# Performance work log

Hardware: AMD Instinct MI355X
Metric: run time of the kernel (lower is better)

## Reference

```python
import jax, jax.numpy as jnp
import numpy as np

B, S, D, H = 4, 2048, 1024, 16
HD = D // H  # head size = 64

def setup_inputs() -> dict:
    key = jax.random.key(0)
    ks = jax.random.split(key, 9)
    s = 1.0 / np.sqrt(D)
    inp = {"x": jax.random.normal(ks[0], (B, S, D), dtype=jnp.float32)}
    for i, n in enumerate(["q", "k", "v", "o"]):
        inp[f"W{n}"] = jax.random.uniform(ks[1 + 2 * i], (D, D), minval=-s, maxval=s, dtype=jnp.float32)
        inp[f"b{n}"] = jax.random.uniform(ks[2 + 2 * i], (D,), minval=-s, maxval=s, dtype=jnp.float32)
    return inp

def reference(x, Wq, bq, Wk, bk, Wv, bv, Wo, bo):
    b, s, d = x.shape
    # project and split heads: [b, h, s, hd]
    def heads(y):
        return y.reshape(b, s, H, HD).transpose(0, 2, 1, 3)
    q = heads(x @ Wq.T + bq)
    k = heads(x @ Wk.T + bk)
    v = heads(x @ Wv.T + bv)
    scores = jnp.einsum('bhqd,bhkd->bhqk', q, k) / jnp.sqrt(jnp.float32(HD))
    attn = jax.nn.softmax(scores, axis=-1)
    ctx = jnp.einsum('bhqk,bhkd->bhqd', attn, v)
    ctx = ctx.transpose(0, 2, 1, 3).reshape(b, s, d)
    return ctx @ Wo.T + bo
```

## Files before the change

### kernel.cpp

```cpp
#include <hip/hip_runtime.h>
#include <hip/hip_bf16.h>

typedef __bf16 bf16;
typedef __bf16 bf16x8 __attribute__((ext_vector_type(8)));
typedef __bf16 bf16x4 __attribute__((ext_vector_type(4)));
typedef float f32x4 __attribute__((ext_vector_type(4)));
typedef float f32x16 __attribute__((ext_vector_type(16)));
typedef unsigned int u32;
typedef u32 u32x4 __attribute__((ext_vector_type(4)));

#define B_ 4
#define S_ 2048
#define D_ 1024
#define H_ 16
#define HD_ 64
#define QKLD 2048
#define LOG2E 1.4426950408889634f

static __device__ __forceinline__ f32x4 mfma16(bf16x8 a, bf16x8 b, f32x4 c) {
  return __builtin_amdgcn_mfma_f32_16x16x32_bf16(a, b, c, 0, 0, 0);
}
static __device__ __forceinline__ f32x16 mfma32(bf16x8 a, bf16x8 b, f32x16 c) {
  return __builtin_amdgcn_mfma_f32_32x32x16_bf16(a, b, c, 0, 0, 0);
}
static __device__ __forceinline__ void gload_lds16(const void* g, void* l) {
  __builtin_amdgcn_global_load_lds(
      (const __attribute__((address_space(1))) void*)g,
      (__attribute__((address_space(3))) void*)l, 16, 0, 0);
}
static __device__ __forceinline__ u32 pack2(float lo, float hi) {
  union { bf16 h[2]; u32 u; } un;
  un.h[0] = (bf16)lo; un.h[1] = (bf16)hi;
  return un.u;
}

__global__ void cvt_kernel(const float* __restrict__ in, bf16* __restrict__ out, int n4) {
  int i = blockIdx.x * blockDim.x + threadIdx.x;
  const int stride = gridDim.x * blockDim.x;
  for (; i < n4; i += stride) {
    float4 v = reinterpret_cast<const float4*>(in)[i];
    bf16x4 o;
    o[0] = (bf16)v.x; o[1] = (bf16)v.y; o[2] = (bf16)v.z; o[3] = (bf16)v.w;
    reinterpret_cast<bf16x4*>(out)[i] = o;
  }
}
__global__ void cvtw_kernel(const float* __restrict__ w0, const float* __restrict__ w1,
                            const float* __restrict__ w2, const float* __restrict__ w3,
                            bf16* __restrict__ o0, bf16* __restrict__ o1,
                            bf16* __restrict__ o2, bf16* __restrict__ o3, int n4) {
  const float* in = blockIdx.y == 0 ? w0 : blockIdx.y == 1 ? w1 : blockIdx.y == 2 ? w2 : w3;
  bf16* out = blockIdx.y == 0 ? o0 : blockIdx.y == 1 ? o1 : blockIdx.y == 2 ? o2 : o3;
  const int i = blockIdx.x * blockDim.x + threadIdx.x;
  float4 v = reinterpret_cast<const float4*>(in)[i];
  bf16x4 o;
  o[0] = (bf16)v.x; o[1] = (bf16)v.y; o[2] = (bf16)v.z; o[3] = (bf16)v.w;
  reinterpret_cast<bf16x4*>(out)[i] = o;
}

template<bool OUT_BF16, bool BIAS_ROW>
__global__ __launch_bounds__(256, 2)
void gemm3(const bf16* __restrict__ A, const bf16* __restrict__ W,
           const float* __restrict__ bias, void* __restrict__ Cout,
           int M, int N, int K, float scale) {
  __shared__ __align__(16) char lds[73728];
  const int tid = threadIdx.x;
  const int wave = tid >> 6;
  const int lane = tid & 63;
  const int g = lane >> 4, r16 = lane & 15;
  const unsigned nwgx = gridDim.x;
  const unsigned nwg = nwgx * gridDim.y;
  unsigned lid = blockIdx.x + nwgx * blockIdx.y;
  unsigned swz = (lid & 7) * (nwg >> 3) + (lid >> 3);
  const int m0 = (int)(swz / nwgx) * 128, n0 = (int)(swz % nwgx) * 256;
  const int wm = (wave >> 1) * 64, wn = (wave & 1) * 128;

  f32x4 acc[4][8] = {};

  const int arow0 = tid >> 2;
  const int acol = ((tid & 3) ^ ((tid >> 3) & 3)) * 8;
  const int wdst = wave * 1024;
  const int nkt = K >> 5;

  auto stage = [&](int bi, int t) {
    char* buf = lds + bi * 24576;
    const int kb = t << 5;
#pragma unroll
    for (int q = 0; q < 2; ++q)
      gload_lds16(&A[(size_t)(m0 + q * 64 + arow0) * K + kb + acol],
                  buf + q * 4096 + wdst);
#pragma unroll
    for (int q = 0; q < 4; ++q)
      gload_lds16(&W[(size_t)(n0 + q * 64 + arow0) * K + kb + acol],
                  buf + 8192 + q * 4096 + wdst);
  };

  stage(0, 0);
  stage(1, 1);
  int cur = 0;

  for (int t = 0; t < nkt; ++t) {
    if (t + 1 < nkt) asm volatile("s_waitcnt vmcnt(6)" ::: "memory");
    else             asm volatile("s_waitcnt vmcnt(0)" ::: "memory");
    __builtin_amdgcn_s_barrier();
    int nx2 = cur + 2; if (nx2 >= 3) nx2 -= 3;
    if (t + 2 < nkt) stage(nx2, t + 2);

    const char* bufA = lds + cur * 24576;
    const char* bufB = bufA + 8192;
    bf16x8 af[4], bfr[8];
#pragma unroll
    for (int i = 0; i < 4; ++i) {
      const int ra = wm + i * 16 + r16;
      af[i] = *reinterpret_cast<const bf16x8*>(
          bufA + ra * 64 + ((g ^ ((ra >> 1) & 3)) << 4));
    }
#pragma unroll
    for (int j = 0; j < 8; ++j) {
      const int rb = wn + j * 16 + r16;
      bfr[j] = *reinterpret_cast<const bf16x8*>(
          bufB + rb * 64 + ((g ^ ((rb >> 1) & 3)) << 4));
    }
    __builtin_amdgcn_s_setprio(1);
#pragma unroll
    for (int i = 0; i < 4; ++i)
#pragma unroll
      for (int j = 0; j < 8; ++j)
        acc[i][j] = mfma16(af[i], bfr[j], acc[i][j]);
    __builtin_amdgcn_s_setprio(0);
    cur = (cur + 1 == 3) ? 0 : cur + 1;
  }

#pragma unroll
  for (int i = 0; i < 4; ++i) {
#pragma unroll
    for (int j = 0; j < 8; ++j) {
      const int col = n0 + wn + j * 16 + r16;
      float bcol = BIAS_ROW ? 0.f : bias[col];
#pragma unroll
      for (int r = 0; r < 4; ++r) {
        const int row = m0 + wm + i * 16 + g * 4 + r;
        const float bv = BIAS_ROW ? bias[row] : bcol;
        const float v = (acc[i][j][r] + bv) * scale;
        if (OUT_BF16)
          reinterpret_cast<bf16*>(Cout)[(size_t)row * N + col] = (bf16)v;
        else
          reinterpret_cast<float*>(Cout)[(size_t)row * N + col] = v;
      }
    }
  }
}

__global__ __launch_bounds__(256, 2)
void gemm_qkv(const bf16* __restrict__ X, const bf16* __restrict__ Wqk,
              const bf16* __restrict__ Wv,
              const float* __restrict__ bq, const float* __restrict__ bk,
              const float* __restrict__ bv,
              bf16* __restrict__ QKout, bf16* __restrict__ VTout) {
  __shared__ __align__(16) char lds[49152];
  const int tid = threadIdx.x;
  const int wave = tid >> 6;
  const int lane = tid & 63;
  const int g = lane >> 4, r16 = lane & 15;
  const int K = 1024;
  const unsigned lid = blockIdx.x;
  const unsigned swz = (lid & 7) * (1536 >> 3) + (lid >> 3);
  const bool isQK = swz < 1024;
  int m0, n0;
  const bf16 *Aptr, *Wptr;
  if (isQK) {
    m0 = (int)(swz >> 4) * 128;
    n0 = (int)(swz & 15) * 128;
    Aptr = X; Wptr = Wqk;
  } else {
    const unsigned v = swz - 1024;
    m0 = (int)(v >> 6) * 128;
    n0 = (int)(v & 63) * 128;
    Aptr = Wv; Wptr = X;
  }
  const int wm = (wave >> 1) * 64, wn = (wave & 1) * 64;

  f32x4 acc[4][4] = {};

  const int nkt = K >> 5;

  auto stage = [&](int bi, int t) {
    char* buf = lds + bi * 16384;
    const int kb = t << 5;
#pragma unroll
    for (int l = 0; l < 2; ++l) {
      const int s = tid + l * 256;
      const int row = s >> 2;
      const int col = ((s & 3) ^ ((s >> 3) & 3)) * 8;
      gload_lds16(&Aptr[(size_t)(m0 + row) * K + kb + col], buf + wave * 1024 + l * 4096);
      gload_lds16(&Wptr[(size_t)(n0 + row) * K + kb + col], buf + 8192 + wave * 1024 + l * 4096);
    }
  };

  stage(0, 0);
  stage(1, 1);
  int cur = 0;

  for (int t = 0; t < nkt; ++t) {
    if (t + 1 < nkt) asm volatile("s_waitcnt vmcnt(4)" ::: "memory");
    else             asm volatile("s_waitcnt vmcnt(0)" ::: "memory");
    __builtin_amdgcn_s_barrier();
    int nx2 = cur + 2; if (nx2 >= 3) nx2 -= 3;
    if (t + 2 < nkt) stage(nx2, t + 2);

    const char* bufA = lds + cur * 16384;
    const char* bufB = bufA + 8192;
    bf16x8 af[4], bfr[4];
#pragma unroll
    for (int i = 0; i < 4; ++i) {
      const int ra = wm + i * 16 + r16;
      af[i] = *reinterpret_cast<const bf16x8*>(
          bufA + ra * 64 + ((g ^ ((ra >> 1) & 3)) << 4));
      const int rb = wn + i * 16 + r16;
      bfr[i] = *reinterpret_cast<const bf16x8*>(
          bufB + rb * 64 + ((g ^ ((rb >> 1) & 3)) << 4));
    }
    __builtin_amdgcn_s_setprio(1);
#pragma unroll
    for (int i = 0; i < 4; ++i)
#pragma unroll
      for (int j = 0; j < 4; ++j)
        acc[i][j] = mfma16(af[i], bfr[j], acc[i][j]);
    __builtin_amdgcn_s_setprio(0);
    cur = (cur + 1 == 3) ? 0 : cur + 1;
  }

  if (isQK) {
#pragma unroll
    for (int i = 0; i < 4; ++i) {
#pragma unroll
      for (int j = 0; j < 4; ++j) {
        const int col = n0 + wn + j * 16 + r16;
        const bool isQ = col < 1024;
        const float bb = isQ ? bq[col] : bk[col - 1024];
        const float sc = isQ ? 0.125f * LOG2E : 1.0f;
#pragma unroll
        for (int r = 0; r < 4; ++r) {
          const int row = m0 + wm + i * 16 + g * 4 + r;
          QKout[(size_t)row * QKLD + col] = (bf16)((acc[i][j][r] + bb) * sc);
        }
      }
    }
  } else {
#pragma unroll
    for (int i = 0; i < 4; ++i) {
#pragma unroll
      for (int j = 0; j < 4; ++j) {
        const int col = n0 + wn + j * 16 + r16;
#pragma unroll
        for (int r = 0; r < 4; ++r) {
          const int row = m0 + wm + i * 16 + g * 4 + r;
          VTout[(size_t)row * (B_ * S_) + col] = (bf16)(acc[i][j][r] + bv[row]);
        }
      }
    }
  }
}

#define VMB(N) do { asm volatile("s_waitcnt vmcnt(" #N ")" ::: "memory"); \
                    __builtin_amdgcn_s_barrier(); } while (0)

__global__ __launch_bounds__(256, 2)
void attn_kernel(const bf16* __restrict__ QK, const bf16* __restrict__ Vt,
                 bf16* __restrict__ CTX) {
  const unsigned nwg = gridDim.x * gridDim.y;
  const unsigned lid = blockIdx.x + gridDim.x * blockIdx.y;
  const unsigned swzid = (lid & 7) * (nwg >> 3) + (lid >> 3);
  const int bh = (int)(swzid >> 3);
  const int q0 = (int)(swzid & 7) * 256;
  const int h = bh & (H_ - 1), b = bh >> 4;
  const int tid = threadIdx.x, wave = tid >> 6, lane = tid & 63;
  const int l32 = lane & 31, hi = lane >> 5;

  const bf16* Qb  = QK + ((size_t)b * S_) * QKLD + h * HD_;
  const bf16* Kb  = QK + ((size_t)b * S_) * QKLD + 1024 + h * HD_;
  const bf16* Vtb = Vt + (size_t)(h * HD_) * (B_ * S_) + b * S_;

  __shared__ __align__(16) char lds[49152];
  char* const kb0 = lds;             char* const vb0 = lds + 24576;
  char* const kb1 = lds + 8192;      char* const vb1 = lds + 32768;
  char* const kb2 = lds + 16384;     char* const vb2 = lds + 40960;

  const int qbase = q0 + wave * 64;
  bf16x8 qf0[4], qf1[4];
#pragma unroll
  for (int ks = 0; ks < 4; ++ks) {
    qf0[ks] = *reinterpret_cast<const bf16x8*>(&Qb[(size_t)(qbase + l32) * QKLD + ks * 16 + hi * 8]);
    qf1[ks] = *reinterpret_cast<const bf16x8*>(&Qb[(size_t)(qbase + 32 + l32) * QKLD + ks * 16 + hi * 8]);
  }

  bf16x8 onesf;
#pragma unroll
  for (int j = 0; j < 8; ++j) onesf[j] = (bf16)1.0f;

  f32x16 ctx00 = {}, ctx01 = {}, ctx10 = {}, ctx11 = {};
  f32x16 lacc0 = {}, lacc1 = {};

  const int krow0 = wave * 16 + (lane >> 3);
  const int xs = ((lane & 7) ^ (lane >> 3)) * 8;
  const int stoff = wave * 2048;
  const int swl = (l32 & 7) << 4;
  int coa[4];
#pragma unroll
  for (int ks = 0; ks < 4; ++ks) coa[ks] = (ks * 32 + hi * 16) ^ swl;
  const int rA = l32 * 128, rB = (32 + l32) * 128;

  const bf16* Kst = Kb  + (size_t)krow0 * QKLD + xs;
  const bf16* Vst = Vtb + (size_t)krow0 * (B_ * S_) + xs;

  auto stage = [&](char* kd, char* vd) {
    gload_lds16(Kst,                  kd + stoff);
    gload_lds16(Kst + 8 * QKLD,       kd + stoff + 1024);
    gload_lds16(Vst,                  vd + stoff);
    gload_lds16(Vst + 8 * (B_ * S_),  vd + stoff + 1024);
    Kst += 64 * QKLD;
    Vst += 64;
  };

  auto expack = [&](const f32x16& s, u32* w) {
#pragma unroll
    for (int a = 0; a < 4; ++a)
#pragma unroll
      for (int c = 0; c < 2; ++c)
        w[2 * a + c] = pack2(__builtin_amdgcn_exp2f(s[4 * a + 2 * c]),
                             __builtin_amdgcn_exp2f(s[4 * a + 2 * c + 1]));
  };

  auto compute = [&](const char* bK, const char* bV) {
    bf16x8 kf0[4], kf1[4];
#pragma unroll
    for (int ks = 0; ks < 4; ++ks) {
      kf0[ks] = *reinterpret_cast<const bf16x8*>(bK + rA + coa[ks]);
      kf1[ks] = *reinterpret_cast<const bf16x8*>(bK + rB + coa[ks]);
    }
    const f32x16 z = {};
    f32x16 s00, s01;
    __builtin_amdgcn_s_setprio(1);
    s00 = mfma32(kf0[0], qf0[0], z);
    s01 = mfma32(kf1[0], qf0[0], z);
#pragma unroll
    for (int ks = 1; ks < 4; ++ks) {
      s00 = mfma32(kf0[ks], qf0[ks], s00);
      s01 = mfma32(kf1[ks], qf0[ks], s01);
    }
    __builtin_amdgcn_s_setprio(0);
    u32 w00[8], w01[8];
    expack(s00, w00); expack(s01, w01);
    f32x16 s10, s11;
    __builtin_amdgcn_s_setprio(1);
    s10 = mfma32(kf0[0], qf1[0], z);
    s11 = mfma32(kf1[0], qf1[0], z);
#pragma unroll
    for (int ks = 1; ks < 4; ++ks) {
      s10 = mfma32(kf0[ks], qf1[ks], s10);
      s11 = mfma32(kf1[ks], qf1[ks], s11);
    }
    __builtin_amdgcn_s_setprio(0);
    u32 w10[8], w11[8];
    expack(s10, w10); expack(s11, w11);
    bf16x8 vf0[4], vf1[4];
#pragma unroll
    for (int ksp = 0; ksp < 4; ++ksp) {
      vf0[ksp] = *reinterpret_cast<const bf16x8*>(bV + rA + coa[ksp]);
      vf1[ksp] = *reinterpret_cast<const bf16x8*>(bV + rB + coa[ksp]);
    }
#pragma unroll
    for (int m = 0; m < 2; ++m) {
      const u32* wlo = m ? w10 : w00;
      const u32* whi = m ? w11 : w01;
      f32x16& la = m ? lacc1 : lacc0;
      f32x16& c0 = m ? ctx10 : ctx00;
      f32x16& c1 = m ? ctx11 : ctx01;
#pragma unroll
      for (int T = 0; T < 2; ++T) {
        const u32* w = T ? whi : wlo;
#pragma unroll
        for (int k1 = 0; k1 < 2; ++k1) {
          auto rAp = __builtin_amdgcn_permlane32_swap((int)w[4 * k1 + 0], (int)w[4 * k1 + 2], false, false);
          auto rBp = __builtin_amdgcn_permlane32_swap((int)w[4 * k1 + 1], (int)w[4 * k1 + 3], false, false);
          u32x4 fw;
          fw[0] = (u32)rAp[0]; fw[1] = (u32)rBp[0]; fw[2] = (u32)rAp[1]; fw[3] = (u32)rBp[1];
          const bf16x8 pa = __builtin_bit_cast(bf16x8, fw);
          const int ksp = 2 * T + k1;
          __builtin_amdgcn_s_setprio(1);
          la = mfma32(pa, onesf, la);
          c0 = mfma32(pa, vf0[ksp], c0);
          c1 = mfma32(pa, vf1[ksp], c1);
          __builtin_amdgcn_s_setprio(0);
        }
      }
    }
  };

  stage(kb0, vb0);
  stage(kb1, vb1);

  for (int u = 0; u < 10; ++u) {
    VMB(4); stage(kb2, vb2); compute(kb0, vb0);
    VMB(4); stage(kb0, vb0); compute(kb1, vb1);
    VMB(4); stage(kb1, vb1); compute(kb2, vb2);
  }
  VMB(4); compute(kb0, vb0);
  VMB(0); compute(kb1, vb1);
  __syncthreads();

  char* Cw = lds + wave * 8192;
#pragma unroll
  for (int rg = 0; rg < 16; ++rg) {
    const int ql = (rg & 3) + 8 * (rg >> 2) + 4 * hi;
    const int swq = (ql & 7) << 4;
    {
      const float inv = 1.0f / lacc0[rg];
      *reinterpret_cast<bf16*>(Cw + ql * 128 + ((l32 * 2) ^ swq)) = (bf16)(ctx00[rg] * inv);
      *reinterpret_cast<bf16*>(Cw + ql * 128 + ((64 + l32 * 2) ^ swq)) = (bf16)(ctx01[rg] * inv);
    }
    {
      const float inv = 1.0f / lacc1[rg];
      *reinterpret_cast<bf16*>(Cw + (32 + ql) * 128 + ((l32 * 2) ^ swq)) = (bf16)(ctx10[rg] * inv);
      *reinterpret_cast<bf16*>(Cw + (32 + ql) * 128 + ((64 + l32 * 2) ^ swq)) = (bf16)(ctx11[rg] * inv);
    }
  }
  asm volatile("" ::: "memory");
#pragma unroll
  for (int i = 0; i < 8; ++i) {
    const int s = i * 64 + lane;
    const int row = s >> 3, cs = (s & 7) * 16;
    bf16x8 v = *reinterpret_cast<const bf16x8*>(Cw + row * 128 + (cs ^ ((row & 7) << 4)));
    *reinterpret_cast<bf16x8*>(
        &CTX[(size_t)(b * S_ + q0 + wave * 64 + row) * D_ + h * HD_ + cs / 2]) = v;
  }
}

extern "C" void kernel_launch(void* const* d_in, const int* in_sizes, int n_in,
                              void* d_out, int out_size, void* d_ws, size_t ws_size,
                              hipStream_t stream) {
  const float* x  = (const float*)d_in[0];
  const float* Wq = (const float*)d_in[1]; const float* bq = (const float*)d_in[2];
  const float* Wk = (const float*)d_in[3]; const float* bk = (const float*)d_in[4];
  const float* Wv = (const float*)d_in[5]; const float* bv = (const float*)d_in[6];
  const float* Wo = (const float*)d_in[7]; const float* bo = (const float*)d_in[8];

  char* ws = (char*)d_ws;
  const size_t MB = 1048576;
  bf16* xb  = (bf16*)(ws);
  bf16* wqb = (bf16*)(ws + 16 * MB);
  bf16* wkb = (bf16*)(ws + 18 * MB);
  bf16* wvb = (bf16*)(ws + 20 * MB);
  bf16* wob = (bf16*)(ws + 22 * MB);
  bf16* qkb = (bf16*)(ws + 24 * MB);
  bf16* vtb = (bf16*)(ws + 56 * MB);
  bf16* ctx = (bf16*)(ws + 72 * MB);

  cvt_kernel<<<2048, 256, 0, stream>>>(x, xb, 2097152);
  cvtw_kernel<<<dim3(1024, 4), 256, 0, stream>>>(Wq, Wk, Wv, Wo, wqb, wkb, wvb, wob, 262144);

  gemm_qkv<<<1536, 256, 0, stream>>>(xb, wqb, wvb, bq, bk, bv, qkb, vtb);

  attn_kernel<<<dim3(8, 64), 256, 0, stream>>>(qkb, vtb, ctx);

  dim3 gq(1024 / 256, 8192 / 128);
  gemm3<false, false><<<gq, 256, 0, stream>>>(ctx, wob, bo, d_out, 8192, 1024, 1024, 1.0f);
}
```

Baseline: 187.3 us.

## Switch attention KV pipeline to double-buffered 128-key stages

Replaces the three-slot, 64-key ring buffer with two 128-key slots, so each stage loads twice as many K/V rows and each barrier covers two compute steps. This is meant to halve the number of barrier and wait points per tile. The loop now waits for all outstanding loads (vmcnt 0) before each barrier, so there is less prefetch depth. LDS use grows from 48 KB to 64 KB per block, which may cut occupancy below the two blocks requested by the launch bounds.

Result: no change. 189.6 us (+1.2%).

```diff
diff --git a/kernel.cpp b/kernel.cpp
--- a/kernel.cpp
+++ b/kernel.cpp
@@ -261,9 +261,6 @@
   }
 }
 
-#define VMB(N) do { asm volatile("s_waitcnt vmcnt(" #N ")" ::: "memory"); \
-                    __builtin_amdgcn_s_barrier(); } while (0)
-
 __global__ __launch_bounds__(256, 2)
 void attn_kernel(const bf16* __restrict__ QK, const bf16* __restrict__ Vt,
                  bf16* __restrict__ CTX) {
@@ -280,10 +277,11 @@
   const bf16* Kb  = QK + ((size_t)b * S_) * QKLD + 1024 + h * HD_;
   const bf16* Vtb = Vt + (size_t)(h * HD_) * (B_ * S_) + b * S_;
 
-  __shared__ __align__(16) char lds[49152];
-  char* const kb0 = lds;             char* const vb0 = lds + 24576;
-  char* const kb1 = lds + 8192;      char* const vb1 = lds + 32768;
-  char* const kb2 = lds + 16384;     char* const vb2 = lds + 40960;
+  __shared__ __align__(16) char lds[65536];
+  char* const kA = lds;
+  char* const kB = lds + 16384;
+  char* const vA = lds + 32768;
+  char* const vB = lds + 49152;
 
   const int qbase = q0 + wave * 64;
   bf16x8 qf0[4], qf1[4];
@@ -313,12 +311,16 @@
   const bf16* Vst = Vtb + (size_t)krow0 * (B_ * S_) + xs;
 
   auto stage = [&](char* kd, char* vd) {
-    gload_lds16(Kst,                  kd + stoff);
-    gload_lds16(Kst + 8 * QKLD,       kd + stoff + 1024);
-    gload_lds16(Vst,                  vd + stoff);
-    gload_lds16(Vst + 8 * (B_ * S_),  vd + stoff + 1024);
-    Kst += 64 * QKLD;
-    Vst += 64;
+    gload_lds16(Kst,                        kd + stoff);
+    gload_lds16(Kst + 8 * QKLD,             kd + stoff + 1024);
+    gload_lds16(Kst + 64 * QKLD,            kd + 8192 + stoff);
+    gload_lds16(Kst + 72 * QKLD,            kd + 8192 + stoff + 1024);
+    gload_lds16(Vst,                        vd + stoff);
+    gload_lds16(Vst + 8 * (B_ * S_),        vd + stoff + 1024);
+    gload_lds16(Vst + 64,                   vd + 8192 + stoff);
+    gload_lds16(Vst + 8 * (B_ * S_) + 64,   vd + 8192 + stoff + 1024);
+    Kst += 128 * QKLD;
+    Vst += 128;
   };
 
   auto expack = [&](const f32x16& s, u32* w) {
@@ -396,16 +398,23 @@
     }
   };
 
-  stage(kb0, vb0);
-  stage(kb1, vb1);
-
-  for (int u = 0; u < 10; ++u) {
-    VMB(4); stage(kb2, vb2); compute(kb0, vb0);
-    VMB(4); stage(kb0, vb0); compute(kb1, vb1);
-    VMB(4); stage(kb1, vb1); compute(kb2, vb2);
-  }
-  VMB(4); compute(kb0, vb0);
-  VMB(0); compute(kb1, vb1);
+  stage(kA, vA);
+  asm volatile("s_waitcnt vmcnt(0)" ::: "memory");
+  __builtin_amdgcn_s_barrier();
+
+  for (int t = 0; t < 15; ++t) {
+    char* kn = (t & 1) ? kA : kB;
+    char* vn = (t & 1) ? vA : vB;
+    stage(kn, vn);
+    const char* kc = (t & 1) ? kB : kA;
+    const char* vc = (t & 1) ? vB : vA;
+    compute(kc, vc);
+    compute(kc + 8192, vc + 8192);
+    asm volatile("s_waitcnt vmcnt(0)" ::: "memory");
+    __builtin_amdgcn_s_barrier();
+  }
+  compute(kB, vB);
+  compute(kB + 8192, vB + 8192);
   __syncthreads();
 
   char* Cw = lds + wave * 8192;
```
